# Kernel tuning notes

Hardware: AMD Instinct MI355X
Metric: run time of the kernel (lower is better)

Reference implementation:

```python
import jax, jax.numpy as jnp
import numpy as np
from jax import lax

CHUNK = 32

def _l2norm(x, eps=1e-6):
    # matches fla l2norm: x / ||x||_2 along last dim
    return x * lax.rsqrt(jnp.sum(x * x, axis=-1, keepdims=True) + eps)

def _delta_rule_chunkwise(q, k, v, beta, chunk=CHUNK):
    b, h, L, dk = q.shape
    dv = v.shape[-1]
    pad = (-L) % chunk
    if pad:
        pw = ((0, 0), (0, 0), (0, pad), (0, 0))
        q = jnp.pad(q, pw); k = jnp.pad(k, pw); v = jnp.pad(v, pw)
        beta = jnp.pad(beta, ((0, 0), (0, 0), (0, pad)))
    Lp = L + pad
    n = Lp // chunk

    q = _l2norm(q)
    k = _l2norm(k)
    v = v * beta[..., None]
    k_beta = k * beta[..., None]

    # [b,h,n,c,d]
    rs = lambda t: t.reshape(b, h, n, chunk, t.shape[-1])
    qc, kc, vc, kbc = rs(q), rs(k), rs(v), rs(k_beta)

    idx = jnp.arange(chunk)
    strict_lower = (idx[:, None] > idx[None, :])           # used for inv
    lower_incl = (idx[:, None] >= idx[None, :])            # used for attn_local

    # inv = -(k_beta k^T), keep strictly-lower part only
    inv = jnp.where(strict_lower, -jnp.einsum('bhnid,bhnjd->bhnij', kbc, kc), 0.0)
    # sequential forward substitution: inv[i,:i] += inv[i,:] @ inv[:,:i]
    for i in range(1, chunk):
        row = inv[..., i, :]                                # [b,h,n,c]
        upd = jnp.einsum('bhnk,bhnkc->bhnc', row, inv)      # contributions from rows < i
        inv = inv.at[..., i, :].add(jnp.where(idx < i, upd, 0.0))
    inv = inv + jnp.eye(chunk, dtype=inv.dtype)

    u = jnp.einsum('bhnij,bhnjd->bhnid', inv, vc)           # [b,h,n,c,dv]
    w = jnp.einsum('bhnij,bhnjd->bhnid', inv, kbc)          # [b,h,n,c,dk]

    S0 = jnp.zeros((b, h, dk, dv), dtype=q.dtype)

    def step(S, blk):
        q_i, k_i, u_i0, w_i = blk
        attn = jnp.where(lower_incl, jnp.einsum('bhid,bhjd->bhij', q_i, k_i), 0.0)
        u_i = u_i0 - jnp.einsum('bhik,bhkd->bhid', w_i, S)
        o = jnp.einsum('bhik,bhkd->bhid', q_i, S) + jnp.einsum('bhij,bhjd->bhid', attn, u_i)
        S = S + jnp.einsum('bhci,bhcd->bhid', k_i, u_i)
        return S, o

    mv = lambda t: jnp.moveaxis(t, 2, 0)                    # [n,b,h,c,d]
    S, outs = lax.scan(step, S0, (mv(qc), mv(kc), mv(u), mv(w)))
    out = jnp.moveaxis(outs, 0, 2).reshape(b, h, Lp, dv)
    if pad:
        out = out[:, :, :L]
    return out, S

def setup_inputs() -> dict:
    key = jax.random.key(0)
    kq, kk, kv, kb = jax.random.split(key, 4)
    b, h, L, d = 2, 16, 4096, 128
    q = jax.random.normal(kq, (b, h, L, d), dtype=jnp.float32)
    k = jax.random.normal(kk, (b, h, L, d), dtype=jnp.float32)
    v = jax.random.normal(kv, (b, h, L, d), dtype=jnp.float32)
    beta = jax.random.uniform(kb, (b, h, L), dtype=jnp.float32)
    return {"q": q, "k": k, "v": v, "beta": beta}

def reference(q, k, v, beta):
    return _delta_rule_chunkwise(q, k, v, beta)
```

## Files before the change

kernel.cpp:

```cpp
#include <hip/hip_runtime.h>
#include <math.h>

#define BH   32
#define LSEQ 4096
#define DK   128
#define DV   128
#define CH   32
#define NC   (LSEQ/CH)

typedef float4 f4;
typedef unsigned short u16;
typedef __attribute__((ext_vector_type(8))) short  bf16x8;
typedef __attribute__((ext_vector_type(4))) float  f32x4;

#define MFMA16(a,b,c) __builtin_amdgcn_mfma_f32_16x16x32_bf16((a),(b),(c),0,0,0)

__device__ __forceinline__ float dot4(const f4 a, const f4 b) {
    return a.x*b.x + a.y*b.y + a.z*b.z + a.w*b.w;
}
__device__ __forceinline__ unsigned pk2(float a, float b) {
    unsigned ua = __builtin_bit_cast(unsigned, a);
    unsigned ub = __builtin_bit_cast(unsigned, b);
    ua = (ua + 0x7FFFu + ((ua >> 16) & 1u)) >> 16;
    ub = (ub + 0x7FFFu + ((ub >> 16) & 1u)) >> 16;
    return (ua & 0xFFFFu) | (ub << 16);
}
__device__ __forceinline__ u16 bf1(float a) {
    unsigned ua = __builtin_bit_cast(unsigned, a);
    ua = (ua + 0x7FFFu + ((ua >> 16) & 1u)) >> 16;
    return (u16)ua;
}

__global__ __launch_bounds__(256) void prep_kernel(
    const float* __restrict__ q, const float* __restrict__ k, float* __restrict__ v,
    const float* __restrict__ beta,
    u16* __restrict__ qb16, u16* __restrict__ wb16,
    u16* __restrict__ kT16, u16* __restrict__ A16)
{
    __shared__ u16 qn[CH][136];
    __shared__ u16 kn[CH][136];
    __shared__ u16 vT[DK][40];
    __shared__ u16 knT[DK][40];
    __shared__ float Ts[CH][33];
    __shared__ float Af[CH][33];
    __shared__ u16 Tb[CH][40];
    __shared__ float redq[CH][8], redk[CH][8];
    __shared__ float bet[CH], scq[CH], sck[CH];

    const int tid = threadIdx.x;
    const int hh  = blockIdx.x >> 7;
    const int c   = blockIdx.x & (NC-1);
    const size_t rowbase = (size_t)hh * LSEQ + (size_t)c * CH;
    const size_t base    = rowbase * DK;
    const size_t tb      = (size_t)(hh * NC + c);

    const int r = tid >> 3, sub = tid & 7, d0 = sub * 16;
    const int wid = tid >> 6, lane = tid & 63, quad = lane >> 4, m16 = lane & 15;

    f4 tq[4], tk[4], tv[4];
    float sq = 0.f, sk = 0.f;
#pragma unroll
    for (int m = 0; m < 4; ++m) {
        tq[m] = *(const f4*)(q + base + (size_t)r*DK + d0 + m*4);
        tk[m] = *(const f4*)(k + base + (size_t)r*DK + d0 + m*4);
        tv[m] = *(const f4*)(v + base + (size_t)r*DK + d0 + m*4);
        sq += dot4(tq[m], tq[m]);
        sk += dot4(tk[m], tk[m]);
    }
    redq[r][sub] = sq;
    redk[r][sub] = sk;
    if (tid < CH) bet[tid] = beta[rowbase + tid];
    __syncthreads();
    if (tid < CH) {
        float a = 0.f, b = 0.f;
#pragma unroll
        for (int j = 0; j < 8; ++j) { a += redq[tid][j]; b += redk[tid][j]; }
        scq[tid] = 1.0f / sqrtf(a + 1e-6f);
        sck[tid] = 1.0f / sqrtf(b + 1e-6f);
    }
    __syncthreads();
    const float aq = scq[r], ak = sck[r];
#pragma unroll
    for (int m = 0; m < 4; ++m) {
        tq[m].x *= aq; tq[m].y *= aq; tq[m].z *= aq; tq[m].w *= aq;
        tk[m].x *= ak; tk[m].y *= ak; tk[m].z *= ak; tk[m].w *= ak;
    }
    {
        uint4 p0, p1;
        p0.x = pk2(tq[0].x,tq[0].y); p0.y = pk2(tq[0].z,tq[0].w);
        p0.z = pk2(tq[1].x,tq[1].y); p0.w = pk2(tq[1].z,tq[1].w);
        p1.x = pk2(tq[2].x,tq[2].y); p1.y = pk2(tq[2].z,tq[2].w);
        p1.z = pk2(tq[3].x,tq[3].y); p1.w = pk2(tq[3].z,tq[3].w);
        *(uint4*)&qn[r][d0]     = p0;  *(uint4*)&qn[r][d0+8] = p1;
        *(uint4*)(qb16 + tb*4096 + (size_t)r*DK + d0)     = p0;
        *(uint4*)(qb16 + tb*4096 + (size_t)r*DK + d0 + 8) = p1;
        uint4 k0, k1;
        k0.x = pk2(tk[0].x,tk[0].y); k0.y = pk2(tk[0].z,tk[0].w);
        k0.z = pk2(tk[1].x,tk[1].y); k0.w = pk2(tk[1].z,tk[1].w);
        k1.x = pk2(tk[2].x,tk[2].y); k1.y = pk2(tk[2].z,tk[2].w);
        k1.z = pk2(tk[3].x,tk[3].y); k1.w = pk2(tk[3].z,tk[3].w);
        *(uint4*)&kn[r][d0]     = k0;  *(uint4*)&kn[r][d0+8] = k1;
    }
#pragma unroll
    for (int m = 0; m < 4; ++m) {
        knT[d0+m*4+0][r] = bf1(tk[m].x); knT[d0+m*4+1][r] = bf1(tk[m].y);
        knT[d0+m*4+2][r] = bf1(tk[m].z); knT[d0+m*4+3][r] = bf1(tk[m].w);
        vT [d0+m*4+0][r] = bf1(tv[m].x); vT [d0+m*4+1][r] = bf1(tv[m].y);
        vT [d0+m*4+2][r] = bf1(tv[m].z); vT [d0+m*4+3][r] = bf1(tv[m].w);
    }
    __syncthreads();

    {
        const int d = tid >> 1, jh = (tid & 1) * 16;
        uint4 z0 = *(const uint4*)&knT[d][jh];
        uint4 z1 = *(const uint4*)&knT[d][jh+8];
        *(uint4*)(kT16 + tb*4096 + (size_t)d*32 + jh)     = z0;
        *(uint4*)(kT16 + tb*4096 + (size_t)d*32 + jh + 8) = z1;
    }
    {
        const int ti = wid >> 1, tj = wid & 1;
        f32x4 aA = {0.f,0.f,0.f,0.f}, aG = {0.f,0.f,0.f,0.f};
#pragma unroll
        for (int ks = 0; ks < 4; ++ks) {
            bf16x8 xq = *(const bf16x8*)&qn[ti*16+m16][ks*32 + quad*8];
            bf16x8 xk = *(const bf16x8*)&kn[ti*16+m16][ks*32 + quad*8];
            bf16x8 yk = *(const bf16x8*)&kn[tj*16+m16][ks*32 + quad*8];
            aA = MFMA16(xq, yk, aA);
            aG = MFMA16(xk, yk, aG);
        }
#pragma unroll
        for (int reg = 0; reg < 4; ++reg) {
            Af[ti*16 + quad*4 + reg][tj*16 + m16] = aA[reg];
            Ts[ti*16 + quad*4 + reg][tj*16 + m16] = aG[reg];
        }
    }
    __syncthreads();

    {
        const int i = r, j0 = sub * 4;
        float a[4];
#pragma unroll
        for (int jj = 0; jj < 4; ++jj)
            a[jj] = (j0+jj <= i) ? Af[i][j0+jj] : 0.f;
        uint2 pa; pa.x = pk2(a[0], a[1]); pa.y = pk2(a[2], a[3]);
        *(uint2*)(A16 + tb*1024 + (size_t)i*32 + j0) = pa;
        const float bi = bet[i];
#pragma unroll
        for (int jj = 0; jj < 4; ++jj) {
            const int j = j0 + jj;
            const float gv = Ts[i][j];
            Ts[i][j] = (j < i) ? -bi * gv : 0.f;
        }
    }
    __syncthreads();

    if (tid < 32) {
        float rr[32];
#pragma unroll
        for (int i = 0; i < 32; ++i) rr[i] = Ts[i][tid];
#pragma unroll
        for (int i = 1; i < 32; ++i) {
            float t = 0.f;
#pragma unroll
            for (int kk = 0; kk < i; ++kk)
                t += __shfl(rr[i], kk) * rr[kk];
            rr[i] += t;
        }
        const float bj = bet[tid];
#pragma unroll
        for (int i = 0; i < 32; ++i)
            Ts[i][tid] = ((i == tid) ? 1.0f : rr[i]) * bj;
    }
    __syncthreads();
    {
        const int i = r, j0 = sub * 4;
        uint2 p; p.x = pk2(Ts[i][j0], Ts[i][j0+1]); p.y = pk2(Ts[i][j0+2], Ts[i][j0+3]);
        *(uint2*)&Tb[i][j0] = p;
    }
    __syncthreads();

#pragma unroll
    for (int dt = 0; dt < 2; ++dt)
#pragma unroll
    for (int it = 0; it < 2; ++it) {
        const int drow = wid*32 + dt*16 + m16;
        bf16x8 av  = *(const bf16x8*)&vT[drow][quad*8];
        bf16x8 ak2 = *(const bf16x8*)&knT[drow][quad*8];
        bf16x8 bT  = *(const bf16x8*)&Tb[it*16 + m16][quad*8];
        f32x4 aU = {0.f,0.f,0.f,0.f}, aW = {0.f,0.f,0.f,0.f};
        aU = MFMA16(av,  bT, aU);
        aW = MFMA16(ak2, bT, aW);
        const int ii = it*16 + m16;
        const int dd = wid*32 + dt*16 + quad*4;
        f4 us; us.x = aU[0]; us.y = aU[1]; us.z = aU[2]; us.w = aU[3];
        *(f4*)(v + base + (size_t)ii*DK + dd) = us;
        uint2 pw; pw.x = pk2(-aW[0], -aW[1]); pw.y = pk2(-aW[2], -aW[3]);
        *(uint2*)(wb16 + tb*4096 + (size_t)ii*DK + dd) = pw;
    }
}

__global__ __launch_bounds__(256, 1) void scan_kernel(
    const u16* __restrict__ qb16, const u16* __restrict__ wb16,
    const u16* __restrict__ kT16, const u16* __restrict__ A16,
    const float* __restrict__ u0, float* __restrict__ out)
{
    __shared__ u16   wbc[2][16][CH][8];
    __shared__ u16   STc[2][16][16][8];
    __shared__ float uIT[2][16][36];

    const int tid  = threadIdx.x;
    const int hh   = blockIdx.x & (BH-1);
    const int g    = blockIdx.x >> 5;
    const int wid  = tid >> 6;
    const int lane = tid & 63;
    const int quad = lane >> 4;
    const int m16  = lane & 15;

    const int srow = tid >> 3;
    const int spl  = (tid & 7) * 2;
    const int um   = (tid & 7) * 2;

    const u16* qg = qb16 + (size_t)hh * NC * 4096;
    const u16* wg = wb16 + (size_t)hh * NC * 4096;
    const u16* kg = kT16 + (size_t)hh * NC * 4096;
    const u16* Ag = A16  + (size_t)hh * NC * 1024;
    const float* ug = u0 + (size_t)hh * LSEQ * DK + g * 16;

    uint4 Ow0, Ow1, Ew0, Ew1; float2 Ou, Eu;
    bf16x8 F0 = {}, F1 = {}, F2 = {}, F3 = {}, AF = {};
    f32x4 S0 = {0.f,0.f,0.f,0.f}, S1 = {0.f,0.f,0.f,0.f};
    f32x4 S2 = {0.f,0.f,0.f,0.f}, S3 = {0.f,0.f,0.f,0.f};

#define PREF(P, cc) do { \
    const u16* wp_ = wg + (size_t)(cc)*4096 + (size_t)srow*DK + (tid&7)*16; \
    P##w0 = *(const uint4*)(wp_); \
    P##w1 = *(const uint4*)(wp_ + 8); \
    P##u  = *(const float2*)(ug + ((size_t)(cc)*CH + srow)*DK + um); \
} while (0)

#define STAGE(P, nb_) do { \
    *(uint4*)&wbc[nb_][spl  ][srow][0] = P##w0; \
    *(uint4*)&wbc[nb_][spl+1][srow][0] = P##w1; \
    uIT[nb_][um  ][srow] = P##u.x; \
    uIT[nb_][um+1][srow] = P##u.y; \
} while (0)

#define LOADFRAGS(cc) do { \
    if (wid < 2) { \
        const u16* kp_ = kg + (size_t)(cc)*4096 + (size_t)(wid*64 + m16)*32 + quad*8; \
        F0 = *(const bf16x8*)(kp_); \
        F1 = *(const bf16x8*)(kp_ + 16*32); \
        F2 = *(const bf16x8*)(kp_ + 32*32); \
        F3 = *(const bf16x8*)(kp_ + 48*32); \
    } else { \
        const u16* qp_ = qg + (size_t)(cc)*4096 + (size_t)((wid-2)*16 + m16)*DK + quad*8; \
        F0 = *(const bf16x8*)(qp_); \
        F1 = *(const bf16x8*)(qp_ + 32); \
        F2 = *(const bf16x8*)(qp_ + 64); \
        F3 = *(const bf16x8*)(qp_ + 96); \
        AF = *(const bf16x8*)(Ag + (size_t)(cc)*1024 + (size_t)((wid-2)*16 + m16)*32 + quad*8); \
    } \
} while (0)

    for (int i = tid; i < 16*16*8; i += 256) (&STc[0][0][0][0])[i] = 0;
    PREF(O, 0);
    STAGE(O, 0);
    PREF(O, 1);
    PREF(E, 2);
    LOADFRAGS(0);
    __syncthreads();

#define BODY(c, b, P) do { \
    const int nb = (b) ^ 1; \
    STAGE(P, nb); \
    { const int c3_ = ((c)+3 < NC) ? (c)+3 : NC-1; PREF(P, c3_); } \
     \
    f32x4 u0a = *(const f32x4*)&uIT[b][m16][quad*4]; \
    f32x4 u1a = *(const f32x4*)&uIT[b][m16][16 + quad*4]; \
    f32x4 u0b = {0.f,0.f,0.f,0.f}, u1b = {0.f,0.f,0.f,0.f}; \
    bf16x8 sf0 = *(const bf16x8*)&STc[b][quad    ][m16][0]; \
    bf16x8 sf1 = *(const bf16x8*)&STc[b][ 4+quad ][m16][0]; \
    bf16x8 sf2 = *(const bf16x8*)&STc[b][ 8+quad ][m16][0]; \
    bf16x8 sf3 = *(const bf16x8*)&STc[b][12+quad ][m16][0]; \
    u0a = MFMA16(*(const bf16x8*)&wbc[b][quad    ][   m16][0], sf0, u0a); \
    u1a = MFMA16(*(const bf16x8*)&wbc[b][quad    ][16+m16][0], sf0, u1a); \
    u0b = MFMA16(*(const bf16x8*)&wbc[b][ 4+quad ][   m16][0], sf1, u0b); \
    u1b = MFMA16(*(const bf16x8*)&wbc[b][ 4+quad ][16+m16][0], sf1, u1b); \
    u0a = MFMA16(*(const bf16x8*)&wbc[b][ 8+quad ][   m16][0], sf2, u0a); \
    u1a = MFMA16(*(const bf16x8*)&wbc[b][ 8+quad ][16+m16][0], sf2, u1a); \
    u0b = MFMA16(*(const bf16x8*)&wbc[b][12+quad ][   m16][0], sf3, u0b); \
    u1b = MFMA16(*(const bf16x8*)&wbc[b][12+quad ][16+m16][0], sf3, u1b); \
    u0a[0]+=u0b[0]; u0a[1]+=u0b[1]; u0a[2]+=u0b[2]; u0a[3]+=u0b[3]; \
    u1a[0]+=u1b[0]; u1a[1]+=u1b[1]; u1a[2]+=u1b[2]; u1a[3]+=u1b[3]; \
     \
    const unsigned W00 = pk2(u0a[0], u0a[1]), W01 = pk2(u0a[2], u0a[3]); \
    const unsigned W10 = pk2(u1a[0], u1a[1]), W11 = pk2(u1a[2], u1a[3]); \
    const int s0l_ = (2*(quad&1))*16 + m16, s1l_ = s0l_ + 16; \
    union { unsigned w[4]; bf16x8 v; } uc_; \
    { const unsigned a0_ = __shfl((int)W00, s0l_), b0_ = __shfl((int)W10, s0l_); \
      const unsigned a1_ = __shfl((int)W01, s0l_), b1_ = __shfl((int)W11, s0l_); \
      const unsigned a2_ = __shfl((int)W00, s1l_), b2_ = __shfl((int)W10, s1l_); \
      const unsigned a3_ = __shfl((int)W01, s1l_), b3_ = __shfl((int)W11, s1l_); \
      const bool hi_ = (quad >= 2); \
      uc_.w[0] = hi_ ? b0_ : a0_; uc_.w[1] = hi_ ? b1_ : a1_; \
      uc_.w[2] = hi_ ? b2_ : a2_; uc_.w[3] = hi_ ? b3_ : a3_; } \
    const bf16x8 ub_ = uc_.v; \
    if (wid < 2) { \
         \
        const int db_ = wid * 64; \
        S0 = MFMA16(F0, ub_, S0); \
        S1 = MFMA16(F1, ub_, S1); \
        S2 = MFMA16(F2, ub_, S2); \
        S3 = MFMA16(F3, ub_, S3); \
        uint2 p_; \
        p_.x = pk2(S0[0],S0[1]); p_.y = pk2(S0[2],S0[3]); \
        *(uint2*)&STc[nb][(db_>>3)   + (quad>>1)][m16][4*(quad&1)] = p_; \
        p_.x = pk2(S1[0],S1[1]); p_.y = pk2(S1[2],S1[3]); \
        *(uint2*)&STc[nb][(db_>>3)+2 + (quad>>1)][m16][4*(quad&1)] = p_; \
        p_.x = pk2(S2[0],S2[1]); p_.y = pk2(S2[2],S2[3]); \
        *(uint2*)&STc[nb][(db_>>3)+4 + (quad>>1)][m16][4*(quad&1)] = p_; \
        p_.x = pk2(S3[0],S3[1]); p_.y = pk2(S3[2],S3[3]); \
        *(uint2*)&STc[nb][(db_>>3)+6 + (quad>>1)][m16][4*(quad&1)] = p_; \
    } else { \
         \
        f32x4 Za = {0.f,0.f,0.f,0.f}, Zb = {0.f,0.f,0.f,0.f}; \
        Za = MFMA16(F0, sf0, Za); \
        Zb = MFMA16(F1, sf1, Zb); \
        Za = MFMA16(F2, sf2, Za); \
        Zb = MFMA16(F3, sf3, Zb); \
        Za[0]+=Zb[0]; Za[1]+=Zb[1]; Za[2]+=Zb[2]; Za[3]+=Zb[3]; \
        Za = MFMA16(AF, ub_, Za); \
        float* op_ = out + ((size_t)hh*LSEQ + (size_t)(c)*CH + (wid-2)*16 + quad*4)*DV \
                         + g*16 + m16; \
        op_[0] = Za[0]; op_[DV] = Za[1]; op_[2*DV] = Za[2]; op_[3*DV] = Za[3]; \
    } \
    { const int c1_ = ((c)+1 < NC) ? (c)+1 : NC-1; LOADFRAGS(c1_); } \
    __syncthreads(); \
} while (0)

    for (int c = 0; c < NC; c += 2) {
        BODY(c,     0, O);
        BODY(c + 1, 1, E);
    }

    if (wid < 2) {
        float* sp = out + (size_t)BH*LSEQ*DV
                        + ((size_t)hh*DK + wid*64 + quad*4)*DV + g*16 + m16;
        sp[0] = S0[0]; sp[DV] = S0[1]; sp[2*DV] = S0[2]; sp[3*DV] = S0[3];
        sp += (size_t)16*DV;
        sp[0] = S1[0]; sp[DV] = S1[1]; sp[2*DV] = S1[2]; sp[3*DV] = S1[3];
        sp += (size_t)16*DV;
        sp[0] = S2[0]; sp[DV] = S2[1]; sp[2*DV] = S2[2]; sp[3*DV] = S2[3];
        sp += (size_t)16*DV;
        sp[0] = S3[0]; sp[DV] = S3[1]; sp[2*DV] = S3[2]; sp[3*DV] = S3[3];
    }
#undef BODY
#undef LOADFRAGS
#undef STAGE
#undef PREF
}

extern "C" void kernel_launch(void* const* d_in, const int* in_sizes, int n_in,
                              void* d_out, int out_size, void* d_ws, size_t ws_size,
                              hipStream_t stream) {
    (void)in_sizes; (void)n_in; (void)out_size; (void)ws_size;
    const float* q = (const float*)d_in[0];
    const float* k = (const float*)d_in[1];
    float* v = (float*)d_in[2];
    const float* beta = (const float*)d_in[3];
    float* out = (float*)d_out;

    const size_t NE = (size_t)BH * LSEQ * DK;
    u16* qb16 = (u16*)d_ws;
    u16* wb16 = qb16 + NE;
    u16* kT16 = wb16 + NE;
    u16* A16  = kT16 + NE;

    prep_kernel<<<dim3(BH*NC), dim3(256), 0, stream>>>(q, k, v, beta, qb16, wb16, kT16, A16);
    scan_kernel<<<dim3(8*BH), dim3(256), 0, stream>>>(qb16, wb16, kT16, A16, v, out);
}
```

Measured before the change: 378.3 us.

## Double-buffer scan fragments, store w pre-tiled, and use LDS-only barrier

The prep kernel now writes the w matrix already in the LDS tile order the scan uses, so staging becomes a contiguous 32-byte copy per thread instead of a strided scatter. The q/k/A fragment registers are doubled (odd/even sets), so global loads are issued two chunks ahead and have a full iteration to arrive. __syncthreads is replaced by a barrier that waits only on LDS counters, so outstanding global prefetches are not drained at each step. This costs extra registers and depends on the hand-written wait being enough for correctness.

```diff
diff --git a/kernel.cpp b/kernel.cpp
--- a/kernel.cpp
+++ b/kernel.cpp
@@ -195,7 +195,7 @@
         f4 us; us.x = aU[0]; us.y = aU[1]; us.z = aU[2]; us.w = aU[3];
         *(f4*)(v + base + (size_t)ii*DK + dd) = us;
         uint2 pw; pw.x = pk2(-aW[0], -aW[1]); pw.y = pk2(-aW[2], -aW[3]);
-        *(uint2*)(wb16 + tb*4096 + (size_t)ii*DK + dd) = pw;
+        *(uint2*)(wb16 + tb*4096 + (size_t)((dd>>3)*256 + ii*8 + (dd&7))) = pw;
     }
 }
 
@@ -204,8 +204,8 @@
     const u16* __restrict__ kT16, const u16* __restrict__ A16,
     const float* __restrict__ u0, float* __restrict__ out)
 {
-    __shared__ u16   wbc[2][16][CH][8];
-    __shared__ u16   STc[2][16][16][8];
+    __shared__ __align__(16) u16   wbc[2][16][CH][8];
+    __shared__ __align__(16) u16   STc[2][16][16][8];
     __shared__ float uIT[2][16][36];
 
     const int tid  = threadIdx.x;
@@ -217,7 +217,6 @@
     const int m16  = lane & 15;
 
     const int srow = tid >> 3;
-    const int spl  = (tid & 7) * 2;
     const int um   = (tid & 7) * 2;
 
     const u16* qg = qb16 + (size_t)hh * NC * 4096;
@@ -227,39 +226,47 @@
     const float* ug = u0 + (size_t)hh * LSEQ * DK + g * 16;
 
     uint4 Ow0, Ow1, Ew0, Ew1; float2 Ou, Eu;
-    bf16x8 F0 = {}, F1 = {}, F2 = {}, F3 = {}, AF = {};
+    bf16x8 OF0 = {}, OF1 = {}, OF2 = {}, OF3 = {}, OAF = {};
+    bf16x8 EF0 = {}, EF1 = {}, EF2 = {}, EF3 = {}, EAF = {};
     f32x4 S0 = {0.f,0.f,0.f,0.f}, S1 = {0.f,0.f,0.f,0.f};
     f32x4 S2 = {0.f,0.f,0.f,0.f}, S3 = {0.f,0.f,0.f,0.f};
 
 #define PREF(P, cc) do { \
-    const u16* wp_ = wg + (size_t)(cc)*4096 + (size_t)srow*DK + (tid&7)*16; \
+    const u16* wp_ = wg + (size_t)(cc)*4096 + (size_t)tid*16; \
     P##w0 = *(const uint4*)(wp_); \
     P##w1 = *(const uint4*)(wp_ + 8); \
     P##u  = *(const float2*)(ug + ((size_t)(cc)*CH + srow)*DK + um); \
 } while (0)
 
 #define STAGE(P, nb_) do { \
-    *(uint4*)&wbc[nb_][spl  ][srow][0] = P##w0; \
-    *(uint4*)&wbc[nb_][spl+1][srow][0] = P##w1; \
+    u16* wl_ = ((u16*)wbc) + (size_t)(nb_)*4096 + (size_t)tid*16; \
+    *(uint4*)(wl_)     = P##w0; \
+    *(uint4*)(wl_ + 8) = P##w1; \
     uIT[nb_][um  ][srow] = P##u.x; \
     uIT[nb_][um+1][srow] = P##u.y; \
 } while (0)
 
-#define LOADFRAGS(cc) do { \
+#define LOADFRAGS(P, cc) do { \
     if (wid < 2) { \
         const u16* kp_ = kg + (size_t)(cc)*4096 + (size_t)(wid*64 + m16)*32 + quad*8; \
-        F0 = *(const bf16x8*)(kp_); \
-        F1 = *(const bf16x8*)(kp_ + 16*32); \
-        F2 = *(const bf16x8*)(kp_ + 32*32); \
-        F3 = *(const bf16x8*)(kp_ + 48*32); \
+        P##F0 = *(const bf16x8*)(kp_); \
+        P##F1 = *(const bf16x8*)(kp_ + 16*32); \
+        P##F2 = *(const bf16x8*)(kp_ + 32*32); \
+        P##F3 = *(const bf16x8*)(kp_ + 48*32); \
     } else { \
         const u16* qp_ = qg + (size_t)(cc)*4096 + (size_t)((wid-2)*16 + m16)*DK + quad*8; \
-        F0 = *(const bf16x8*)(qp_); \
-        F1 = *(const bf16x8*)(qp_ + 32); \
-        F2 = *(const bf16x8*)(qp_ + 64); \
-        F3 = *(const bf16x8*)(qp_ + 96); \
-        AF = *(const bf16x8*)(Ag + (size_t)(cc)*1024 + (size_t)((wid-2)*16 + m16)*32 + quad*8); \
+        P##F0 = *(const bf16x8*)(qp_); \
+        P##F1 = *(const bf16x8*)(qp_ + 32); \
+        P##F2 = *(const bf16x8*)(qp_ + 64); \
+        P##F3 = *(const bf16x8*)(qp_ + 96); \
+        P##AF = *(const bf16x8*)(Ag + (size_t)(cc)*1024 + (size_t)((wid-2)*16 + m16)*32 + quad*8); \
     } \
+} while (0)
+
+#define RAWBAR() do { \
+    asm volatile("s_waitcnt lgkmcnt(0)" ::: "memory"); \
+    __builtin_amdgcn_s_barrier(); \
+    __builtin_amdgcn_sched_barrier(0); \
 } while (0)
 
     for (int i = tid; i < 16*16*8; i += 256) (&STc[0][0][0][0])[i] = 0;
@@ -267,8 +274,9 @@
     STAGE(O, 0);
     PREF(O, 1);
     PREF(E, 2);
-    LOADFRAGS(0);
-    __syncthreads();
+    LOADFRAGS(O, 0);
+    LOADFRAGS(E, 1);
+    RAWBAR();
 
 #define BODY(c, b, P) do { \
     const int nb = (b) ^ 1; \
@@ -308,10 +316,10 @@
     if (wid < 2) { \
          \
         const int db_ = wid * 64; \
-        S0 = MFMA16(F0, ub_, S0); \
-        S1 = MFMA16(F1, ub_, S1); \
-        S2 = MFMA16(F2, ub_, S2); \
-        S3 = MFMA16(F3, ub_, S3); \
+        S0 = MFMA16(P##F0, ub_, S0); \
+        S1 = MFMA16(P##F1, ub_, S1); \
+        S2 = MFMA16(P##F2, ub_, S2); \
+        S3 = MFMA16(P##F3, ub_, S3); \
         uint2 p_; \
         p_.x = pk2(S0[0],S0[1]); p_.y = pk2(S0[2],S0[3]); \
         *(uint2*)&STc[nb][(db_>>3)   + (quad>>1)][m16][4*(quad&1)] = p_; \
@@ -324,18 +332,19 @@
     } else { \
          \
         f32x4 Za = {0.f,0.f,0.f,0.f}, Zb = {0.f,0.f,0.f,0.f}; \
-        Za = MFMA16(F0, sf0, Za); \
-        Zb = MFMA16(F1, sf1, Zb); \
-        Za = MFMA16(F2, sf2, Za); \
-        Zb = MFMA16(F3, sf3, Zb); \
+        Za = MFMA16(P##F0, sf0, Za); \
+        Zb = MFMA16(P##F1, sf1, Zb); \
+        Za = MFMA16(P##F2, sf2, Za); \
+        Zb = MFMA16(P##F3, sf3, Zb); \
         Za[0]+=Zb[0]; Za[1]+=Zb[1]; Za[2]+=Zb[2]; Za[3]+=Zb[3]; \
-        Za = MFMA16(AF, ub_, Za); \
+        Za = MFMA16(P##AF, ub_, Za); \
         float* op_ = out + ((size_t)hh*LSEQ + (size_t)(c)*CH + (wid-2)*16 + quad*4)*DV \
                          + g*16 + m16; \
         op_[0] = Za[0]; op_[DV] = Za[1]; op_[2*DV] = Za[2]; op_[3*DV] = Za[3]; \
     } \
-    { const int c1_ = ((c)+1 < NC) ? (c)+1 : NC-1; LOADFRAGS(c1_); } \
-    __syncthreads(); \
+     \
+    { const int c2_ = ((c)+2 < NC) ? (c)+2 : NC-1; LOADFRAGS(P, c2_); } \
+    RAWBAR(); \
 } while (0)
 
     for (int c = 0; c < NC; c += 2) {
@@ -355,6 +364,7 @@
         sp[0] = S3[0]; sp[DV] = S3[1]; sp[2*DV] = S3[2]; sp[3*DV] = S3[3];
     }
 #undef BODY
+#undef RAWBAR
 #undef LOADFRAGS
 #undef STAGE
 #undef PREF
```

After: 355.7 us. 1.06x faster.
